# Kernel optimization log

Hardware: AMD Instinct MI355X
Metric: run time of the kernel (lower is better)

Reference implementation:

```python
import jax, jax.numpy as jnp
import numpy as np

N_QUBITS = 14
N_LAYERS = 3
BATCH = 256


def _apply_1q(state, U, q, n):
    # state: (B, 2^n) flat; apply 2x2 gate U on qubit q.
    # U: (2,2) shared or (B,2,2) per-sample.
    B = state.shape[0]
    s = state.reshape(B, 2 ** q, 2, 2 ** (n - 1 - q))
    if U.ndim == 3:
        s = jnp.einsum('bij,bajc->baic', U, s)
    else:
        s = jnp.einsum('ij,bajc->baic', U, s)
    return s.reshape(B, -1)


def _apply_cnot(state, c, t, n):
    # CNOT: |c, t> -> |c, t xor c>. Flip target axis on the control=1 block.
    B = state.shape[0]
    a, b = (c, t) if c < t else (t, c)
    s = state.reshape(B, 2 ** a, 2, 2 ** (b - a - 1), 2, 2 ** (n - 1 - b))
    c_ax = 2 if c < t else 4
    t_ax = 4 if c < t else 2
    s0 = jax.lax.index_in_dim(s, 0, axis=c_ax, keepdims=False)
    s1 = jax.lax.index_in_dim(s, 1, axis=c_ax, keepdims=False)
    t_ax2 = t_ax if t_ax < c_ax else t_ax - 1
    s1 = jnp.flip(s1, axis=t_ax2)
    s = jnp.stack([s0, s1], axis=c_ax)
    return s.reshape(B, -1)


def _circuit(x, weights, n, L):
    # angles constrained to (-pi, pi) as in the torch wrapper
    angles = jnp.tanh(x) * jnp.float32(np.pi)  # (B, n)
    B = x.shape[0]
    state = jnp.zeros((B, 2 ** n), jnp.complex64).at[:, 0].set(1.0)
    # AngleEmbedding with RY rotations (per-sample gate matrices)
    for q in range(n):
        th = angles[:, q] * 0.5
        c, s = jnp.cos(th), jnp.sin(th)
        U = jnp.stack([jnp.stack([c, -s], -1), jnp.stack([s, c], -1)], -2)
        state = _apply_1q(state, U.astype(jnp.complex64), q, n)
    # BasicEntanglerLayers: per layer, RX(w) on each wire then CNOT ring
    for l in range(L):
        for q in range(n):
            th = weights[l, q] * 0.5
            c = jnp.cos(th).astype(jnp.complex64)
            s = jnp.sin(th).astype(jnp.complex64)
            mis = jnp.complex64(-1j) * s
            U = jnp.stack([jnp.stack([c, mis]), jnp.stack([mis, c])])
            state = _apply_1q(state, U, q, n)
        num_cnots = n if n > 2 else (1 if n == 2 else 0)
        for q in range(num_cnots):
            state = _apply_cnot(state, q, (q + 1) % n, n)
    # <Z_q> = P(q=0) - P(q=1)
    p = (jnp.abs(state) ** 2).reshape((B,) + (2,) * n)  # float32 probs
    expvals = []
    for q in range(n):
        pq = jnp.sum(p, axis=tuple(a for a in range(1, n + 1) if a != q + 1))
        expvals.append(pq[:, 0] - pq[:, 1])
    return jnp.stack(expvals, axis=-1)  # (B, n)


def setup_inputs() -> dict:
    key = jax.random.key(0)
    kx, kw = jax.random.split(key)
    x = jax.random.normal(kx, (BATCH, N_QUBITS), jnp.float32)
    # TorchLayer default init for BasicEntanglerLayers: uniform in [0, 2*pi)
    weights = jax.random.uniform(kw, (N_LAYERS, N_QUBITS), jnp.float32, 0.0, 2.0 * np.pi)
    return {"x": x, "weights": weights}


def reference(x, weights):
    return _circuit(x, weights, N_QUBITS, N_LAYERS)
```

## Files before the change

kernel.cpp:

```cpp
#include <hip/hip_runtime.h>
#include <math.h>

#define NQ 14
#define DIM (1 << NQ)
#define NT 512
#define TA 32
#define NW (NT / 64)
#define PDIM (DIM + DIM / 32)

template <int J> struct IC { static constexpr int v = J; };
template <int N, typename F>
__device__ __forceinline__ void sfor(F&& f) {
    if constexpr (N > 0) { sfor<N - 1>(f); f(IC<N - 1>{}); }
}

typedef float cf2 __attribute__((ext_vector_type(2)));

__device__ __forceinline__ cf2 pk_mul_c(cf2 cs, cf2 a) {
    cf2 t;
    asm("v_pk_mul_f32 %0, %1, %2 op_sel:[0,0] op_sel_hi:[0,1]"
        : "=v"(t) : "v"(cs), "v"(a));
    return t;
}
__device__ __forceinline__ cf2 pk_mul_s(cf2 cs, cf2 a) {
    cf2 t;
    asm("v_pk_mul_f32 %0, %1, %2 op_sel:[1,0] op_sel_hi:[1,1]"
        : "=v"(t) : "v"(cs), "v"(a));
    return t;
}
__device__ __forceinline__ cf2 pk_mul_s_swapneg(cf2 cs, cf2 a) {
    cf2 t;
    asm("v_pk_mul_f32 %0, %1, %2 op_sel:[1,1] op_sel_hi:[1,0] neg_hi:[0,1]"
        : "=v"(t) : "v"(cs), "v"(a));
    return t;
}
__device__ __forceinline__ cf2 pk_fma_c(cf2 cs, cf2 a, cf2 b) {
    cf2 d;
    asm("v_pk_fma_f32 %0, %1, %2, %3 op_sel:[0,0,0] op_sel_hi:[0,1,1]"
        : "=v"(d) : "v"(cs), "v"(a), "v"(b));
    return d;
}
__device__ __forceinline__ cf2 pk_fma_s(cf2 cs, cf2 a, cf2 b) {
    cf2 d;
    asm("v_pk_fma_f32 %0, %1, %2, %3 op_sel:[1,0,0] op_sel_hi:[1,1,1]"
        : "=v"(d) : "v"(cs), "v"(a), "v"(b));
    return d;
}
__device__ __forceinline__ cf2 pk_fma_c_nb(cf2 cs, cf2 a, cf2 b) {
    cf2 d;
    asm("v_pk_fma_f32 %0, %1, %2, %3 op_sel:[0,0,0] op_sel_hi:[0,1,1] neg_lo:[0,0,1] neg_hi:[0,0,1]"
        : "=v"(d) : "v"(cs), "v"(a), "v"(b));
    return d;
}

struct St {
    cf2 a0, a1, a2, a3, a4, a5, a6, a7, a8, a9, a10, a11, a12, a13, a14, a15,
        a16, a17, a18, a19, a20, a21, a22, a23, a24, a25, a26, a27, a28, a29, a30, a31;
};
template <int J> __device__ __forceinline__ cf2& amp(St& s);
#define AMP_GET(J) template <> __device__ __forceinline__ cf2& amp<J>(St& s) { return s.a##J; }
AMP_GET(0)  AMP_GET(1)  AMP_GET(2)  AMP_GET(3)  AMP_GET(4)  AMP_GET(5)  AMP_GET(6)  AMP_GET(7)
AMP_GET(8)  AMP_GET(9)  AMP_GET(10) AMP_GET(11) AMP_GET(12) AMP_GET(13) AMP_GET(14) AMP_GET(15)
AMP_GET(16) AMP_GET(17) AMP_GET(18) AMP_GET(19) AMP_GET(20) AMP_GET(21) AMP_GET(22) AMP_GET(23)
AMP_GET(24) AMP_GET(25) AMP_GET(26) AMP_GET(27) AMP_GET(28) AMP_GET(29) AMP_GET(30) AMP_GET(31)

__host__ __device__ constexpr int pad(int idx) { return idx + (idx >> 5); }

template <int P0, int P1, int P2, int P3, int P4>
struct Tile5 {
    static constexpr int PMASK = (1 << P0) | (1 << P1) | (1 << P2) | (1 << P3) | (1 << P4);
    static __device__ __forceinline__ int base_idx(int t) {
        int idx = 0, tb = 0;
#pragma unroll
        for (int p = 0; p < NQ; ++p)
            if (!((PMASK >> p) & 1)) { idx |= ((t >> tb) & 1) << p; ++tb; }
        return idx;
    }
    static constexpr int off(int j) {
        return ((j & 1) << P0) | (((j >> 1) & 1) << P1) | (((j >> 2) & 1) << P2) |
               (((j >> 3) & 1) << P3) | (((j >> 4) & 1) << P4);
    }
    static constexpr int poff(int j) { return pad(off(j)); }
};

using TL1 = Tile5<9, 10, 11, 12, 13>;
using TL2 = Tile5<5, 6, 7, 8, 9>;
using TL3 = Tile5<1, 2, 3, 4, 5>;
using TL4 = Tile5<0, 1, 13, 12, 11>;
using TT1 = Tile5<9, 10, 11, 12, 13>;
using TT2 = Tile5<4, 5, 6, 7, 8>;
using TT3 = Tile5<13, 0, 1, 2, 3>;

template <class T>
__device__ __forceinline__ void load_tile(const cf2* s, int pb, St& st) {
    sfor<TA>([&](auto jc) {
        constexpr int j = decltype(jc)::v;
        amp<j>(st) = s[pb + T::poff(j)];
    });
}
template <class T>
__device__ __forceinline__ void load_tile_fold(const cf2* s, int pbLo, int pbHi, St& st) {
    sfor<TA>([&](auto jc) {
        constexpr int j = decltype(jc)::v;
        amp<j>(st) = s[((j & 16) ? pbHi : pbLo) + T::poff(j)];
    });
}
template <class T>
__device__ __forceinline__ void store_tile(cf2* s, int pb, St& st) {
    sfor<TA>([&](auto jc) {
        constexpr int j = decltype(jc)::v;
        s[pb + T::poff(j)] = amp<j>(st);
    });
}

template <int LB>
__device__ __forceinline__ void g_ry(St& st, cf2 cs) {
    sfor<TA>([&](auto jc) {
        constexpr int j = decltype(jc)::v;
        if constexpr (!(j & (1 << LB))) {
            constexpr int k = j | (1 << LB);
            cf2 aj = amp<j>(st), ak = amp<k>(st);
            amp<j>(st) = pk_fma_c_nb(cs, aj, pk_mul_s(cs, ak));
            amp<k>(st) = pk_fma_s(cs, aj, pk_mul_c(cs, ak));
        }
    });
}
template <int LB>
__device__ __forceinline__ void g_rx(St& st, cf2 cs) {
    sfor<TA>([&](auto jc) {
        constexpr int j = decltype(jc)::v;
        if constexpr (!(j & (1 << LB))) {
            constexpr int k = j | (1 << LB);
            cf2 aj = amp<j>(st), ak = amp<k>(st);
            amp<j>(st) = pk_fma_c(cs, aj, pk_mul_s_swapneg(cs, ak));
            amp<k>(st) = pk_fma_c(cs, ak, pk_mul_s_swapneg(cs, aj));
        }
    });
}
template <int LC, int LT>
__device__ __forceinline__ void g_cnot(St& st) {
    sfor<TA>([&](auto jc) {
        constexpr int j = decltype(jc)::v;
        if constexpr (((j >> LC) & 1) && !((j >> LT) & 1)) {
            constexpr int k = j | (1 << LT);
            cf2 t = amp<j>(st);
            amp<j>(st) = amp<k>(st);
            amp<k>(st) = t;
        }
    });
}

__global__ void __launch_bounds__(NT) qsim_kernel(const float* __restrict__ x,
                                                  const float* __restrict__ w,
                                                  float* __restrict__ out) {
    __shared__ cf2 sSt[PDIM];
    __shared__ cf2 sCS[56];
    __shared__ float sRed[NW][NQ];

    const int tid = threadIdx.x;
    const int b = blockIdx.x;

    if (tid < 14) {
        float th = tanhf(x[b * NQ + tid]) * 1.57079632679489662f;
        cf2 v; v.x = cosf(th); v.y = sinf(th);
        sCS[tid] = v;
    } else if (tid < 56) {
        float th = w[tid - 14] * 0.5f;
        cf2 v; v.x = cosf(th); v.y = sinf(th);
        sCS[tid] = v;
    }

    const int pbL1 = pad(TL1::base_idx(tid));
    const int pbL2 = pad(TL2::base_idx(tid));
    const int pbL3 = pad(TL3::base_idx(tid));
    const int pbL4 = pad(TL4::base_idx(tid));
    const int pbT2 = pad(TT2::base_idx(tid));
    const int pbT3 = pad(TT3::base_idx(tid));
    const int d2 = ((tid >> 4) & 1) ? 264 : 0;
    const int pbT2lo = pbT2 + d2, pbT2hi = pbT2 - d2;
    const int d3 = (tid & 1) ? 8 : 0;
    const int pbT3lo = pbT3 + d3, pbT3hi = pbT3 - d3;

    __syncthreads();

    St st;

    {
        sfor<TA>([&](auto jc) {
            constexpr int j = decltype(jc)::v;
            cf2 z; z.x = 0.f; z.y = 0.f;
            amp<j>(st) = z;
        });
        if (tid == 0) amp<0>(st).x = 1.f;
        g_ry<0>(st, sCS[4]); g_ry<1>(st, sCS[3]); g_ry<2>(st, sCS[2]);
        g_ry<3>(st, sCS[1]); g_ry<4>(st, sCS[0]);
        g_rx<0>(st, sCS[18]); g_rx<1>(st, sCS[17]); g_rx<2>(st, sCS[16]);
        g_rx<3>(st, sCS[15]); g_rx<4>(st, sCS[14]);
        g_cnot<4, 3>(st); g_cnot<3, 2>(st); g_cnot<2, 1>(st); g_cnot<1, 0>(st);
        store_tile<TL1>(sSt, pbL1, st);
    }
    __syncthreads();
    {
        cf2 y5 = sCS[5], y6 = sCS[6], y7 = sCS[7], y8 = sCS[8];
        cf2 x5 = sCS[19], x6 = sCS[20], x7 = sCS[21], x8 = sCS[22];
        load_tile<TL2>(sSt, pbL2, st);
        g_ry<0>(st, y8); g_ry<1>(st, y7); g_ry<2>(st, y6); g_ry<3>(st, y5);
        g_rx<0>(st, x8); g_rx<1>(st, x7); g_rx<2>(st, x6); g_rx<3>(st, x5);
        g_cnot<4, 3>(st); g_cnot<3, 2>(st); g_cnot<2, 1>(st); g_cnot<1, 0>(st);
        store_tile<TL2>(sSt, pbL2, st);
    }
    __syncthreads();
    {
        cf2 y9 = sCS[9], yA = sCS[10], yB = sCS[11], yC = sCS[12];
        cf2 x9 = sCS[23], xA = sCS[24], xB = sCS[25], xC = sCS[26];
        load_tile<TL3>(sSt, pbL3, st);
        g_ry<0>(st, yC); g_ry<1>(st, yB); g_ry<2>(st, yA); g_ry<3>(st, y9);
        g_rx<0>(st, xC); g_rx<1>(st, xB); g_rx<2>(st, xA); g_rx<3>(st, x9);
        g_cnot<4, 3>(st); g_cnot<3, 2>(st); g_cnot<2, 1>(st); g_cnot<1, 0>(st);
        store_tile<TL3>(sSt, pbL3, st);
    }
    __syncthreads();
    {
        cf2 yD = sCS[13], xD = sCS[27];
        load_tile<TL4>(sSt, pbL4, st);
        g_ry<0>(st, yD);
        g_rx<0>(st, xD);
        g_cnot<1, 0>(st); g_cnot<0, 2>(st);
        store_tile<TL4>(sSt, pbL4, st);
    }
    __syncthreads();

#pragma unroll 1
    for (int l = 1; l < 3; ++l) {
        const int s0 = 14 + l * NQ;
        {
            cf2 c0 = sCS[s0 + 0], c1 = sCS[s0 + 1], c2 = sCS[s0 + 2];
            cf2 c3 = sCS[s0 + 3], c4 = sCS[s0 + 4];
            load_tile<TT1>(sSt, pbL1, st);
            g_rx<0>(st, c4); g_rx<1>(st, c3); g_rx<2>(st, c2);
            g_rx<3>(st, c1); g_rx<4>(st, c0);
            g_cnot<4, 3>(st); g_cnot<3, 2>(st); g_cnot<2, 1>(st); g_cnot<1, 0>(st);
            store_tile<TT1>(sSt, pbL1, st);
        }
        __syncthreads();
        {
            cf2 c5 = sCS[s0 + 5], c6 = sCS[s0 + 6], c7 = sCS[s0 + 7];
            cf2 c8 = sCS[s0 + 8], c9 = sCS[s0 + 9];
            load_tile_fold<TT2>(sSt, pbT2lo, pbT2hi, st);
            g_rx<0>(st, c9); g_rx<1>(st, c8); g_rx<2>(st, c7);
            g_rx<3>(st, c6); g_rx<4>(st, c5);
            g_cnot<4, 3>(st); g_cnot<3, 2>(st); g_cnot<2, 1>(st); g_cnot<1, 0>(st);
            store_tile<TT2>(sSt, pbT2, st);
        }
        __syncthreads();
        {
            cf2 cA = sCS[s0 + 10], cB = sCS[s0 + 11], cC = sCS[s0 + 12], cD = sCS[s0 + 13];
            load_tile_fold<TT3>(sSt, pbT3lo, pbT3hi, st);
            g_rx<1>(st, cD); g_rx<2>(st, cC); g_rx<3>(st, cB); g_rx<4>(st, cA);
            g_cnot<4, 3>(st); g_cnot<3, 2>(st); g_cnot<2, 1>(st); g_cnot<1, 0>(st);
            if (l == 1) store_tile<TT3>(sSt, pbT3, st);
        }
        if (l == 1) __syncthreads();
    }

    float Stot = 0.f, S0 = 0.f, S1 = 0.f, S2 = 0.f, S3 = 0.f, S4 = 0.f;
    sfor<TA>([&](auto jc) {
        constexpr int j = decltype(jc)::v;
        cf2 v = amp<j>(st);
        float pj = v.x * v.x + v.y * v.y;
        Stot += pj;
        S0 += (j & 1)  ? -pj : pj;
        S1 += (j & 2)  ? -pj : pj;
        S2 += (j & 4)  ? -pj : pj;
        S3 += (j & 8)  ? -pj : pj;
        S4 += (j & 16) ? -pj : pj;
    });
    float ev[NQ];
    ev[0] = S0; ev[10] = S4; ev[11] = S3; ev[12] = S2; ev[13] = S1;
#pragma unroll
    for (int q = 1; q <= 9; ++q)
        ev[q] = ((tid >> (9 - q)) & 1) ? -Stot : Stot;

#pragma unroll
    for (int q = 0; q < NQ; ++q) {
#pragma unroll
        for (int o = 32; o > 0; o >>= 1) ev[q] += __shfl_down(ev[q], o);
    }
    const int wv = tid >> 6, ln = tid & 63;
    if (ln == 0) {
#pragma unroll
        for (int q = 0; q < NQ; ++q) sRed[wv][q] = ev[q];
    }
    __syncthreads();
    if (tid < NQ) {
        float acc = 0.f;
#pragma unroll
        for (int k = 0; k < NW; ++k) acc += sRed[k][tid];
        out[b * NQ + tid] = acc;
    }
}

extern "C" void kernel_launch(void* const* d_in, const int* in_sizes, int n_in,
                              void* d_out, int out_size, void* d_ws, size_t ws_size,
                              hipStream_t stream) {
    const float* x = (const float*)d_in[0];
    const float* w = (const float*)d_in[1];
    float* out = (float*)d_out;
    qsim_kernel<<<256, NT, 0, stream>>>(x, w, out);
}
```

Baseline: 79.58 us.

## Fuse first layer into three tile passes with predicated boundary CNOTs

Layer one of the circuit used to run in four shared-memory passes with its own tile layouts. It now reuses the TT1/TT2/TT3 tilings of the later layers, so it needs only three passes. The CNOTs whose control qubit falls outside the tile (4→5 and 9→10) become per-thread predicated swaps, keyed on thread-index bits. This removes one load/store round trip and one block barrier, at the cost of extra select instructions in registers.

```diff
diff --git a/kernel.cpp b/kernel.cpp
--- a/kernel.cpp
+++ b/kernel.cpp
@@ -83,10 +83,6 @@
     static constexpr int poff(int j) { return pad(off(j)); }
 };
 
-using TL1 = Tile5<9, 10, 11, 12, 13>;
-using TL2 = Tile5<5, 6, 7, 8, 9>;
-using TL3 = Tile5<1, 2, 3, 4, 5>;
-using TL4 = Tile5<0, 1, 13, 12, 11>;
 using TT1 = Tile5<9, 10, 11, 12, 13>;
 using TT2 = Tile5<4, 5, 6, 7, 8>;
 using TT3 = Tile5<13, 0, 1, 2, 3>;
@@ -146,6 +142,18 @@
             cf2 t = amp<j>(st);
             amp<j>(st) = amp<k>(st);
             amp<k>(st) = t;
+        }
+    });
+}
+template <int LT>
+__device__ __forceinline__ void g_cnot_pred(St& st, bool ctrl) {
+    sfor<TA>([&](auto jc) {
+        constexpr int j = decltype(jc)::v;
+        if constexpr (!((j >> LT) & 1)) {
+            constexpr int k = j | (1 << LT);
+            cf2 a = amp<j>(st), b = amp<k>(st);
+            amp<j>(st) = ctrl ? b : a;
+            amp<k>(st) = ctrl ? a : b;
         }
     });
 }
@@ -170,16 +178,16 @@
         sCS[tid] = v;
     }
 
-    const int pbL1 = pad(TL1::base_idx(tid));
-    const int pbL2 = pad(TL2::base_idx(tid));
-    const int pbL3 = pad(TL3::base_idx(tid));
-    const int pbL4 = pad(TL4::base_idx(tid));
+    const int pbT1 = pad(TT1::base_idx(tid));
     const int pbT2 = pad(TT2::base_idx(tid));
     const int pbT3 = pad(TT3::base_idx(tid));
     const int d2 = ((tid >> 4) & 1) ? 264 : 0;
     const int pbT2lo = pbT2 + d2, pbT2hi = pbT2 - d2;
     const int d3 = (tid & 1) ? 8 : 0;
     const int pbT3lo = pbT3 + d3, pbT3hi = pbT3 - d3;
+
+    const bool c45 = (tid >> 4) & 1;
+    const bool c9A = tid & 1;
 
     __syncthreads();
 
@@ -197,36 +205,29 @@
         g_rx<0>(st, sCS[18]); g_rx<1>(st, sCS[17]); g_rx<2>(st, sCS[16]);
         g_rx<3>(st, sCS[15]); g_rx<4>(st, sCS[14]);
         g_cnot<4, 3>(st); g_cnot<3, 2>(st); g_cnot<2, 1>(st); g_cnot<1, 0>(st);
-        store_tile<TL1>(sSt, pbL1, st);
+        store_tile<TT1>(sSt, pbT1, st);
     }
     __syncthreads();
     {
-        cf2 y5 = sCS[5], y6 = sCS[6], y7 = sCS[7], y8 = sCS[8];
-        cf2 x5 = sCS[19], x6 = sCS[20], x7 = sCS[21], x8 = sCS[22];
-        load_tile<TL2>(sSt, pbL2, st);
-        g_ry<0>(st, y8); g_ry<1>(st, y7); g_ry<2>(st, y6); g_ry<3>(st, y5);
-        g_rx<0>(st, x8); g_rx<1>(st, x7); g_rx<2>(st, x6); g_rx<3>(st, x5);
+        cf2 y5 = sCS[5], y6 = sCS[6], y7 = sCS[7], y8 = sCS[8], y9 = sCS[9];
+        cf2 x5 = sCS[19], x6 = sCS[20], x7 = sCS[21], x8 = sCS[22], x9 = sCS[23];
+        load_tile<TT2>(sSt, pbT2, st);
+        g_ry<0>(st, y9); g_ry<1>(st, y8); g_ry<2>(st, y7); g_ry<3>(st, y6); g_ry<4>(st, y5);
+        g_rx<0>(st, x9); g_rx<1>(st, x8); g_rx<2>(st, x7); g_rx<3>(st, x6); g_rx<4>(st, x5);
+        g_cnot_pred<4>(st, c45);
         g_cnot<4, 3>(st); g_cnot<3, 2>(st); g_cnot<2, 1>(st); g_cnot<1, 0>(st);
-        store_tile<TL2>(sSt, pbL2, st);
+        store_tile<TT2>(sSt, pbT2, st);
     }
     __syncthreads();
     {
-        cf2 y9 = sCS[9], yA = sCS[10], yB = sCS[11], yC = sCS[12];
-        cf2 x9 = sCS[23], xA = sCS[24], xB = sCS[25], xC = sCS[26];
-        load_tile<TL3>(sSt, pbL3, st);
-        g_ry<0>(st, yC); g_ry<1>(st, yB); g_ry<2>(st, yA); g_ry<3>(st, y9);
-        g_rx<0>(st, xC); g_rx<1>(st, xB); g_rx<2>(st, xA); g_rx<3>(st, x9);
+        cf2 yA = sCS[10], yB = sCS[11], yC = sCS[12], yD = sCS[13];
+        cf2 xA = sCS[24], xB = sCS[25], xC = sCS[26], xD = sCS[27];
+        load_tile<TT3>(sSt, pbT3, st);
+        g_ry<1>(st, yD); g_ry<2>(st, yC); g_ry<3>(st, yB); g_ry<4>(st, yA);
+        g_rx<1>(st, xD); g_rx<2>(st, xC); g_rx<3>(st, xB); g_rx<4>(st, xA);
+        g_cnot_pred<4>(st, c9A);
         g_cnot<4, 3>(st); g_cnot<3, 2>(st); g_cnot<2, 1>(st); g_cnot<1, 0>(st);
-        store_tile<TL3>(sSt, pbL3, st);
-    }
-    __syncthreads();
-    {
-        cf2 yD = sCS[13], xD = sCS[27];
-        load_tile<TL4>(sSt, pbL4, st);
-        g_ry<0>(st, yD);
-        g_rx<0>(st, xD);
-        g_cnot<1, 0>(st); g_cnot<0, 2>(st);
-        store_tile<TL4>(sSt, pbL4, st);
+        store_tile<TT3>(sSt, pbT3, st);
     }
     __syncthreads();
 
@@ -236,11 +237,11 @@
         {
             cf2 c0 = sCS[s0 + 0], c1 = sCS[s0 + 1], c2 = sCS[s0 + 2];
             cf2 c3 = sCS[s0 + 3], c4 = sCS[s0 + 4];
-            load_tile<TT1>(sSt, pbL1, st);
+            load_tile<TT1>(sSt, pbT1, st);
             g_rx<0>(st, c4); g_rx<1>(st, c3); g_rx<2>(st, c2);
             g_rx<3>(st, c1); g_rx<4>(st, c0);
             g_cnot<4, 3>(st); g_cnot<3, 2>(st); g_cnot<2, 1>(st); g_cnot<1, 0>(st);
-            store_tile<TT1>(sSt, pbL1, st);
+            store_tile<TT1>(sSt, pbT1, st);
         }
         __syncthreads();
         {
```

New measurement: 78.19 us. No clear change (-1.7%).
